# Optimization experiments

Measured on AMD Instinct MI355X. Metric: run time of the kernel, lower is better.

Reference implementation:

```python
import jax, jax.numpy as jnp
import numpy as np


def _gru_cell(x, h, W_ih, W_hh, b_ih, b_hh):
    # torch.nn.GRUCell semantics, gate order (r, z, n)
    gi = x @ W_ih.T + b_ih          # [B, 3H]
    gh = h @ W_hh.T + b_hh          # [B, 3H]
    ir, iz, inn = jnp.split(gi, 3, axis=-1)
    hr, hz, hn = jnp.split(gh, 3, axis=-1)
    r = jax.nn.sigmoid(ir + hr)
    z = jax.nn.sigmoid(iz + hz)
    n = jnp.tanh(inn + r * hn)
    return (1.0 - z) * n + z * h


def setup_inputs() -> dict:
    key = jax.random.key(0)
    ks = jax.random.split(key, 9)
    B, T, X, H = 128, 512, 64, 256
    s = 0.05
    return {
        "input": jax.random.normal(ks[0], (B, T, X), jnp.float32),
        "h_enc": jax.random.normal(ks[1], (B, H), jnp.float32),
        "W_ih": jax.random.normal(ks[2], (3 * H, X), jnp.float32) * s,
        "W_hh": jax.random.normal(ks[3], (3 * H, H), jnp.float32) * s,
        "b_ih": jnp.zeros((3 * H,), jnp.float32),
        "b_hh": jnp.zeros((3 * H,), jnp.float32),
        "W_out": jax.random.normal(ks[4], (X, H), jnp.float32) * s,
        "b_out": jnp.zeros((X,), jnp.float32),
        "mask0": jax.random.randint(ks[5], (T,), 0, 2, jnp.int32),
        "mask1": jax.random.randint(ks[6], (T,), 0, 2, jnp.int32),
        "skip_size": 4,
    }


def _skip_tables(T, skip):
    # Replicates Python-list negative indexing of the original forward.
    # Skip-list position at the GRU call (pre-append):  2i   if i<skip else i-skip
    # Skip-list position at the projection (post-append): 2i+1 if i<skip else i-skip
    # Positions < skip are zero placeholders; position p >= skip is H[p-skip].
    g_idx = np.zeros(T, np.int32); g_zero = np.zeros(T, bool)
    p_idx = np.zeros(T, np.int32); p_zero = np.zeros(T, bool)
    for i in range(T):
        pg = 2 * i if i < skip else i - skip
        pp = 2 * i + 1 if i < skip else i - skip
        g_zero[i] = pg < skip; g_idx[i] = max(pg - skip, 0)
        p_zero[i] = pp < skip; p_idx[i] = max(pp - skip, 0)
    return g_idx, g_zero, p_idx, p_zero


def reference(input, h_enc, W_ih, W_hh, b_ih, b_hh, W_out, b_out, mask0, mask1, skip_size):
    B, T, X = input.shape
    H = h_enc.shape[1]
    g_idx, g_zero, p_idx, p_zero = _skip_tables(T, int(skip_size))
    m0 = mask0.astype(input.dtype)
    m1 = mask1.astype(input.dtype)

    xs = (jnp.arange(T), m0, m1,
          jnp.asarray(g_idx), jnp.asarray(g_zero),
          jnp.asarray(p_idx), jnp.asarray(p_zero))

    def step(carry, sx):
        h_prev, x_prev, buf = carry          # buf: [T, B, H] history of GRU outputs
        i, a0, a1, gi, gz, pi, pz = sx
        skip_g = jnp.where(gz, 0.0, buf[gi])            # [B, H]
        hidden = h_prev * a0 + skip_g * a1
        h_new = _gru_cell(x_prev, hidden, W_ih, W_hh, b_ih, b_hh)
        buf = buf.at[i].set(h_new)                       # append H[i]
        skip_p = jnp.where(pz, 0.0, buf[pi])
        out = (h_prev + skip_p) @ W_out.T + b_out        # [B, X]
        return (h_new, out, buf), out

    buf0 = jnp.zeros((T, B, H), input.dtype)
    go = jnp.zeros((B, X), input.dtype)                  # GO token
    (_, _, _), outs = jax.lax.scan(step, (h_enc, go, buf0), xs)
    return jnp.transpose(outs, (1, 0, 2))                # [B, T, X]
```

## Files before the change

kernel.cpp:

```cpp
#include <hip/hip_runtime.h>

typedef _Float16 h2_t __attribute__((ext_vector_type(2)));

constexpr int T_ = 512;
constexpr int X_ = 64;
constexpr int H_ = 256;
constexpr int NWG = 128;
constexpr int NT = 512;
constexpr int RS = 16;

constexpr int G_TOTAL = 64 * NT;

__device__ __forceinline__ float sigmoid_f(float x) {
  float e = __expf(fminf(-x, 80.f));
  return 1.f / (1.f + e);
}
__device__ __forceinline__ float tanh_f(float x) {
  float e = __expf(fminf(-2.f * x, 80.f));
  return (1.f - e) / (1.f + e);
}

__device__ __forceinline__ unsigned pk2(float a, float b) {
  h2_t v;
  v[0] = (_Float16)a;
  v[1] = (_Float16)b;
  return __builtin_bit_cast(unsigned, v);
}
__device__ __forceinline__ uint4 pk8(const float* s) {
  return make_uint4(pk2(s[0], s[1]), pk2(s[2], s[3]), pk2(s[4], s[5]),
                    pk2(s[6], s[7]));
}

__device__ __forceinline__ float dotp(unsigned w, unsigned h, float acc) {
  h2_t wv = __builtin_bit_cast(h2_t, w);
  h2_t hv = __builtin_bit_cast(h2_t, h);
#if __has_builtin(__builtin_amdgcn_fdot2)
  return __builtin_amdgcn_fdot2(wv, hv, acc, false);
#else
  acc = fmaf((float)wv[0], (float)hv[0], acc);
  return fmaf((float)wv[1], (float)hv[1], acc);
#endif
}
__device__ __forceinline__ float dotq(uint4 w, uint4 h, float acc) {
  acc = dotp(w.x, h.x, acc);
  acc = dotp(w.y, h.y, acc);
  acc = dotp(w.z, h.z, acc);
  acc = dotp(w.w, h.w, acc);
  return acc;
}

__device__ __forceinline__ float dpp_xor1(float x) {
  int v = __builtin_amdgcn_update_dpp(0, __builtin_bit_cast(int, x), 0xB1,
                                      0xF, 0xF, true);
  return __builtin_bit_cast(float, v);
}
__device__ __forceinline__ float dpp_xor2(float x) {
  int v = __builtin_amdgcn_update_dpp(0, __builtin_bit_cast(int, x), 0x4E,
                                      0xF, 0xF, true);
  return __builtin_bit_cast(float, v);
}

__device__ __forceinline__ void bar_lds() {
  asm volatile("s_waitcnt lgkmcnt(0)\n\ts_barrier" ::: "memory");
}

__global__ void prep_kernel(const float* __restrict__ Wih,
                            const float* __restrict__ Whh,
                            const float* __restrict__ Wout,
                            uint4* __restrict__ G) {
  int id = blockIdx.x * 256 + threadIdx.x;
  if (id >= G_TOTAL) return;
  int t = id & (NT - 1), u = id >> 9;
  int c = t >> 1, kh = t & 1;
  if (u < 32) {
    int g = u >> 4, j = u & 15;
    G[id] = pk8(Whh + (size_t)(g * 256 + c) * H_ + kh * 128 + j * 8);
  } else if (u < 48) {
    int j = u - 32;
    G[id] = pk8(Whh + (size_t)(512 + c) * H_ + kh * 128 + j * 8);
  } else if (u < 60) {
    int v = u - 48, g = v >> 2, j = v & 3;
    G[id] = pk8(Wih + (size_t)(g * 256 + c) * X_ + kh * 32 + j * 8);
  } else {
    int j = u - 60, xc = t >> 3, sl = t & 7;
    G[id] = pk8(Wout + (size_t)xc * H_ + sl * 32 + j * 8);
  }
}

#define PTW(cp) (((cp) >> 4) * 36 + ((cp)&15))
#define HIW(w) ((w) + (((w) >> 6) << 2))


#define GATES(p, i, hn)                                                      \
  float hn;                                                                  \
  {                                                                          \
    float a0 = 0, a1 = 0, z0 = 0, z1 = 0, n0 = 0, n1 = 0, ni = 0;            \
    const uint4* h4 = ((const uint4*)hid2[p]) + kh * 17;                     \
    _Pragma("unroll") for (int j = 0; j < 16; j += 2) {                      \
      uint4 ha = h4[j], hb = h4[j + 1];       \
      uint4 wna = wn4[j * NT + t], wnb = wn4[(j + 1) * NT + t];              \
      a0 = dotq(whh_rz[j], ha, a0);                                          \
      a1 = dotq(whh_rz[j + 1], hb, a1);                                      \
      z0 = dotq(whh_rz[16 + j], ha, z0);                                     \
      z1 = dotq(whh_rz[17 + j], hb, z1);                                     \
      n0 = dotq(wna, ha, n0);                                                \
      n1 = dotq(wnb, hb, n1);                                                \
    }                                                                        \
    const uint4* x4 = ((const uint4*)xt2[p]) + kh * 4;                       \
    _Pragma("unroll") for (int j = 0; j < 4; ++j) {                          \
      uint4 xa = x4[j];                                                      \
      a0 = dotq(wih[j], xa, a0);                                             \
      z0 = dotq(wih[4 + j], xa, z0);                                         \
      ni = dotq(wih[8 + j], xa, ni);                                         \
    }                                                                        \
    float ar = a0 + a1, az = z0 + z1, anh = n0 + n1;                         \
    ar += dpp_xor1(ar);                                                      \
    az += dpp_xor1(az);                                                      \
    anh += dpp_xor1(anh);                                                    \
    ni += dpp_xor1(ni);                                                      \
    float r = sigmoid_f(ar + bsr);                                           \
    float z = sigmoid_f(az + bsz);                                           \
    float n = tanh_f(ni + bin_ + r * (anh + bhn_));                          \
    hn = fmaf(z, hid_reg - n, n);                    \
    if (kh == 0) ring[(i) & (RS - 1)][c] = hn;                               \
  }

#define PROJ_FIN(q, i)                                                       \
  {                                                                          \
    fa += dpp_xor1(fa);                                                      \
    fa += dpp_xor2(fa);                                                      \
    fa += __shfl_xor(fa, 4);                                                 \
    float o = fa + bo;                                                       \
    if (sl == 0) out[ob + (size_t)(i)*X_ + xc] = o;                          \
    float oo = __shfl_xor(o, 8);                                             \
    if ((t & 15) == 0) xt2[q][t >> 4] = pk2(o, oo);                          \
  }

#define PROJ(p, q, i)                                                        \
  {                                                                          \
    float fa = 0;                                                            \
    const uint4* p4 = (const uint4*)&pt2[p][sl * 36];                        \
    _Pragma("unroll") for (int j = 0; j < 4; ++j) fa =                       \
        dotq(wout[j], p4[j], fa);                                            \
    PROJ_FIN(q, i)                                                           \
  }

#define MSTEP(i, p, q)                                                       \
  {                                                                          \
    float fa = 0;                                                            \
    const uint4* p4 = (const uint4*)&pt2[p][sl * 36];                        \
    _Pragma("unroll") for (int j = 0; j < 4; ++j) fa =                       \
        dotq(wout[j], p4[j], fa);                                            \
    GATES(p, i, hn)                                                          \
    PROJ_FIN(q, i)                                                           \
    if ((i) + 1 < T_) {                                                      \
      float sgp = ring[((i) + 1 - 2 * skip) & (RS - 1)][c];                  \
      float hidn = m0f[(i) + 1] * hn + m1f[(i) + 1] * sgp;                   \
      float ptn = hn + sgp;                                                  \
      hid_reg = hidn;                                                        \
      float ho = dpp_xor2(hidn);                                             \
      float po = dpp_xor2(ptn);                                              \
      if ((t & 3) == 0) {                                                    \
        int w = t >> 2;                                                      \
        hid2[q][HIW(w)] = pk2(hidn, ho);                                     \
        pt2[q][PTW(w)] = pk2(ptn, po);                                       \
      }                                                                      \
    }                                                                        \
    bar_lds();                                                               \
  }

__global__ __attribute__((amdgpu_flat_work_group_size(NT, NT),
                          amdgpu_waves_per_eu(2, 2))) void decoder_kernel(
    const float* __restrict__ h_enc, const float* __restrict__ b_ih,
    const float* __restrict__ b_hh, const float* __restrict__ b_out,
    const int* __restrict__ mask0, const int* __restrict__ mask1,
    const int* __restrict__ skipp, const uint4* __restrict__ G,
    float* __restrict__ out) {
  __shared__ alignas(16) uint4 wn4[16 * NT];
  __shared__ float ring[RS][H_];
  __shared__ alignas(16) unsigned hid2[2][136];
  __shared__ alignas(16) unsigned pt2[2][8 * 36];
  __shared__ alignas(16) unsigned xt2[2][X_ / 2];
  __shared__ float m0f[T_], m1f[T_];

  const int t = threadIdx.x;
  const int b = blockIdx.x;
  const int c = t >> 1, kh = t & 1;
  const int xc = t >> 3, sl = t & 7;
  const size_t ob = (size_t)b * T_ * X_;

  uint4 whh_rz[32];
  uint4 wih[12];
  uint4 wout[4];
#pragma unroll
  for (int u = 0; u < 32; ++u) whh_rz[u] = G[u * NT + t];
#pragma unroll
  for (int u = 0; u < 12; ++u) wih[u] = G[(48 + u) * NT + t];
#pragma unroll
  for (int u = 0; u < 4; ++u) wout[u] = G[(60 + u) * NT + t];

#pragma unroll
  for (int u = 0; u < 16; ++u) wn4[u * NT + t] = G[(32 + u) * NT + t];
  m0f[t] = (float)mask0[t];
  m1f[t] = (float)mask1[t];

  const int skip = skipp[0];
  const int i0 = (skip == 0) ? T_ : ((2 * skip < T_) ? 2 * skip : T_);

  const float bsr = b_ih[c] + b_hh[c];
  const float bsz = b_ih[H_ + c] + b_hh[H_ + c];
  const float bin_ = b_ih[2 * H_ + c];
  const float bhn_ = b_hh[2 * H_ + c];
  const float bo = b_out[xc];

  float hp = h_enc[(size_t)b * H_ + c];
  float hid_reg = (float)mask0[0] * hp;
  float hps_reg = hp;
  {
    float ho = dpp_xor2(hid_reg);
    if ((t & 3) == 0) hid2[0][HIW(t >> 2)] = pk2(hid_reg, ho);
  }
  if (t < X_ / 2) xt2[0][t] = 0u;
  __syncthreads();

  for (int i = 0; i < i0; ++i) {
    const int p = i & 1, q = p ^ 1;
    GATES(p, i, hn)
    {
      int ppos = (i < skip) ? 2 * i + 1 : i - skip;
      bool pz = ppos < skip;
      int pi = ppos - skip;
      if (pi < 0) pi = 0;
      float sp = pz ? 0.f : ((pi == i) ? hn : ring[pi & (RS - 1)][c]);
      float ptv = hps_reg + sp;
      float po = dpp_xor2(ptv);
      if ((t & 3) == 0) pt2[p][PTW(t >> 2)] = pk2(ptv, po);
    }
    if (i + 1 < T_) {
      int i1 = i + 1;
      int pg = (i1 < skip) ? 2 * i1 : i1 - skip;
      bool gz = pg < skip;
      int gi = pg - skip;
      if (gi < 0) gi = 0;
      if (gi >= i1) gz = true;
      float sg = gz ? 0.f : ((gi == i) ? hn : ring[gi & (RS - 1)][c]);
      float hidn = m0f[i1] * hn + m1f[i1] * sg;
      hid_reg = hidn;
      float ho = dpp_xor2(hidn);
      if ((t & 3) == 0) hid2[q][HIW(t >> 2)] = pk2(hidn, ho);
      if (skip > 0 && i1 >= 2 * skip) {
        float sgp = ring[(i1 - 2 * skip) & (RS - 1)][c];
        float ptn = hn + sgp;
        float po2 = dpp_xor2(ptn);
        if ((t & 3) == 0) pt2[q][PTW(t >> 2)] = pk2(ptn, po2);
      }
    }
    hps_reg = hn;
    __syncthreads();
    PROJ(p, q, i)
    __syncthreads();
  }

#pragma unroll 1
  for (int i = i0; i < T_; i += 2) {
    MSTEP(i, 0, 1)
    MSTEP(i + 1, 1, 0)
  }
}

extern "C" void kernel_launch(void* const* d_in, const int* in_sizes, int n_in,
                              void* d_out, int out_size, void* d_ws,
                              size_t ws_size, hipStream_t stream) {
  (void)in_sizes; (void)n_in; (void)out_size; (void)ws_size;
  const float* h_enc = (const float*)d_in[1];
  const float* W_ih = (const float*)d_in[2];
  const float* W_hh = (const float*)d_in[3];
  const float* b_ih = (const float*)d_in[4];
  const float* b_hh = (const float*)d_in[5];
  const float* W_out = (const float*)d_in[6];
  const float* b_out = (const float*)d_in[7];
  const int* mask0 = (const int*)d_in[8];
  const int* mask1 = (const int*)d_in[9];
  const int* skipp = (const int*)d_in[10];
  float* out = (float*)d_out;
  uint4* G = (uint4*)d_ws;

  prep_kernel<<<dim3(G_TOTAL / 256), dim3(256), 0, stream>>>(W_ih, W_hh,
                                                             W_out, G);
  decoder_kernel<<<dim3(NWG), dim3(NT), 0, stream>>>(
      h_enc, b_ih, b_hh, b_out, mask0, mask1, skipp, G, out);
}
```

Measured before the change: 1.077 ms.

## Double block size to 1024 threads with four-way K-split per hidden unit

Result: slower. 1.187 ms (+10.2%).

```diff
diff --git a/kernel.cpp b/kernel.cpp
--- a/kernel.cpp
+++ b/kernel.cpp
@@ -6,10 +6,10 @@
 constexpr int X_ = 64;
 constexpr int H_ = 256;
 constexpr int NWG = 128;
-constexpr int NT = 512;
+constexpr int NT = 1024;
 constexpr int RS = 16;
 
-constexpr int G_TOTAL = 64 * NT;
+constexpr int G_TOTAL = 32 * NT;
 
 __device__ __forceinline__ float sigmoid_f(float x) {
   float e = __expf(fminf(-x, 80.f));
@@ -59,6 +59,9 @@
                                       0xF, 0xF, true);
   return __builtin_bit_cast(float, v);
 }
+#define QRED(v)                                                              \
+  v += dpp_xor1(v);                                                          \
+  v += dpp_xor2(v);
 
 __device__ __forceinline__ void bar_lds() {
   asm volatile("s_waitcnt lgkmcnt(0)\n\ts_barrier" ::: "memory");
@@ -70,59 +73,64 @@
                             uint4* __restrict__ G) {
   int id = blockIdx.x * 256 + threadIdx.x;
   if (id >= G_TOTAL) return;
-  int t = id & (NT - 1), u = id >> 9;
-  int c = t >> 1, kh = t & 1;
-  if (u < 32) {
-    int g = u >> 4, j = u & 15;
-    G[id] = pk8(Whh + (size_t)(g * 256 + c) * H_ + kh * 128 + j * 8);
-  } else if (u < 48) {
-    int j = u - 32;
-    G[id] = pk8(Whh + (size_t)(512 + c) * H_ + kh * 128 + j * 8);
-  } else if (u < 60) {
-    int v = u - 48, g = v >> 2, j = v & 3;
-    G[id] = pk8(Wih + (size_t)(g * 256 + c) * X_ + kh * 32 + j * 8);
+  int t = id & (NT - 1), u = id >> 10;
+  int c = t >> 2, kq = t & 3;
+  if (u < 16) {
+    int g = u >> 3, j = u & 7;
+    G[id] = pk8(Whh + (size_t)(g * 256 + c) * H_ + kq * 64 + j * 8);
+  } else if (u < 24) {
+    int j = u - 16;
+    G[id] = pk8(Whh + (size_t)(512 + c) * H_ + kq * 64 + j * 8);
+  } else if (u < 30) {
+    int v = u - 24, g = v >> 1, j = v & 1;
+    G[id] = pk8(Wih + (size_t)(g * 256 + c) * X_ + kq * 16 + j * 8);
   } else {
-    int j = u - 60, xc = t >> 3, sl = t & 7;
-    G[id] = pk8(Wout + (size_t)xc * H_ + sl * 32 + j * 8);
-  }
-}
-
-#define PTW(cp) (((cp) >> 4) * 36 + ((cp)&15))
-#define HIW(w) ((w) + (((w) >> 6) << 2))
-
-
-#define GATES(p, i, hn)                                                      \
-  float hn;                                                                  \
-  {                                                                          \
-    float a0 = 0, a1 = 0, z0 = 0, z1 = 0, n0 = 0, n1 = 0, ni = 0;            \
-    const uint4* h4 = ((const uint4*)hid2[p]) + kh * 17;                     \
-    _Pragma("unroll") for (int j = 0; j < 16; j += 2) {                      \
-      uint4 ha = h4[j], hb = h4[j + 1];       \
-      uint4 wna = wn4[j * NT + t], wnb = wn4[(j + 1) * NT + t];              \
-      a0 = dotq(whh_rz[j], ha, a0);                                          \
-      a1 = dotq(whh_rz[j + 1], hb, a1);                                      \
-      z0 = dotq(whh_rz[16 + j], ha, z0);                                     \
-      z1 = dotq(whh_rz[17 + j], hb, z1);                                     \
-      n0 = dotq(wna, ha, n0);                                                \
-      n1 = dotq(wnb, hb, n1);                                                \
+    int j = u - 30, xc = t >> 4, sl = t & 15;
+    G[id] = pk8(Wout + (size_t)xc * H_ + sl * 16 + j * 8);
+  }
+}
+
+#define HW_(k) (((k) >> 6) * 36 + (((k)&63) >> 1))
+#define XW_(k) (((k) >> 4) * 12 + (((k)&15) >> 1))
+
+
+#define GATES_BODY(p, i)                                                     \
+  {                                                                          \
+    float ar = 0, az = 0, an = 0, ni = 0;                                    \
+    const uint4* h4 = ((const uint4*)hid4[p]) + kq * 9;                      \
+    _Pragma("unroll") for (int j = 0; j < 8; ++j) {                          \
+      uint4 hj = h4[j];                                                      \
+      uint4 wnj = wn[j * NT + t];                                            \
+      ar = dotq(wrz[j], hj, ar);                                             \
+      az = dotq(wrz[8 + j], hj, az);                                         \
+      an = dotq(wnj, hj, an);                                                \
     }                                                                        \
-    const uint4* x4 = ((const uint4*)xt2[p]) + kh * 4;                       \
-    _Pragma("unroll") for (int j = 0; j < 4; ++j) {                          \
-      uint4 xa = x4[j];                                                      \
-      a0 = dotq(wih[j], xa, a0);                                             \
-      z0 = dotq(wih[4 + j], xa, z0);                                         \
-      ni = dotq(wih[8 + j], xa, ni);                                         \
+    const uint4* x4 = ((const uint4*)xt4[p]) + kq * 3;                       \
+    {                                                                        \
+      uint4 xa = x4[0], xb = x4[1];                                          \
+      ar = dotq(wih[0], xa, ar);                                             \
+      ar = dotq(wih[1], xb, ar);                                             \
+      az = dotq(wih[2], xa, az);                                             \
+      az = dotq(wih[3], xb, az);                                             \
+      ni = dotq(wih[4], xa, ni);                                             \
+      ni = dotq(wih[5], xb, ni);                                             \
     }                                                                        \
-    float ar = a0 + a1, az = z0 + z1, anh = n0 + n1;                         \
-    ar += dpp_xor1(ar);                                                      \
-    az += dpp_xor1(az);                                                      \
-    anh += dpp_xor1(anh);                                                    \
-    ni += dpp_xor1(ni);                                                      \
+    QRED(ar)                                                                 \
+    QRED(az)                                                                 \
+    QRED(an)                                                                 \
+    QRED(ni)                                                                 \
     float r = sigmoid_f(ar + bsr);                                           \
     float z = sigmoid_f(az + bsz);                                           \
-    float n = tanh_f(ni + bin_ + r * (anh + bhn_));                          \
+    float n = tanh_f(ni + bin_ + r * (an + bhn_));                           \
     hn = fmaf(z, hid_reg - n, n);                    \
-    if (kh == 0) ring[(i) & (RS - 1)][c] = hn;                               \
+    if ((t & 3) == 0) ring[(i) & (RS - 1)][c] = hn;                          \
+  }
+
+#define PROJ_DOTS_BODY(p)                                                    \
+  {                                                                          \
+    const uint4* p4 = (const uint4*)&pt2[p][sl * 12];                        \
+    fa = dotq(wout[0], p4[0], 0.f);                                          \
+    fa = dotq(wout[1], p4[1], fa);                                           \
   }
 
 #define PROJ_FIN(q, i)                                                       \
@@ -130,79 +138,70 @@
     fa += dpp_xor1(fa);                                                      \
     fa += dpp_xor2(fa);                                                      \
     fa += __shfl_xor(fa, 4);                                                 \
+    fa += __shfl_xor(fa, 8);                                                 \
     float o = fa + bo;                                                       \
-    if (sl == 0) out[ob + (size_t)(i)*X_ + xc] = o;                          \
-    float oo = __shfl_xor(o, 8);                                             \
-    if ((t & 15) == 0) xt2[q][t >> 4] = pk2(o, oo);                          \
-  }
-
-#define PROJ(p, q, i)                                                        \
-  {                                                                          \
-    float fa = 0;                                                            \
-    const uint4* p4 = (const uint4*)&pt2[p][sl * 36];                        \
-    _Pragma("unroll") for (int j = 0; j < 4; ++j) fa =                       \
-        dotq(wout[j], p4[j], fa);                                            \
-    PROJ_FIN(q, i)                                                           \
+    if ((t & 15) == 0) out[ob + (size_t)(i)*X_ + xc] = o;                    \
+    float oo = __shfl_xor(o, 16);                                            \
+    if ((t & 31) == 0) xt4[q][XW_(xc)] = pk2(o, oo);                         \
   }
 
 #define MSTEP(i, p, q)                                                       \
   {                                                                          \
-    float fa = 0;                                                            \
-    const uint4* p4 = (const uint4*)&pt2[p][sl * 36];                        \
-    _Pragma("unroll") for (int j = 0; j < 4; ++j) fa =                       \
-        dotq(wout[j], p4[j], fa);                                            \
-    GATES(p, i, hn)                                                          \
+    float hn, fa;                                                            \
+    PROJ_DOTS_BODY(p)                                                        \
+    GATES_BODY(p, i)                                                         \
     PROJ_FIN(q, i)                                                           \
     if ((i) + 1 < T_) {                                                      \
-      float sgp = ring[((i) + 1 - 2 * skip) & (RS - 1)][c];                  \
-      float hidn = m0f[(i) + 1] * hn + m1f[(i) + 1] * sgp;                   \
-      float ptn = hn + sgp;                                                  \
+      float sg = ring[((i) + 1 - 2 * skip) & (RS - 1)][c];                   \
+      float hidn = m0f[(i) + 1] * hn + m1f[(i) + 1] * sg;                    \
+      float ptn = hn + sg;                                                   \
       hid_reg = hidn;                                                        \
-      float ho = dpp_xor2(hidn);                                             \
-      float po = dpp_xor2(ptn);                                              \
-      if ((t & 3) == 0) {                                                    \
-        int w = t >> 2;                                                      \
-        hid2[q][HIW(w)] = pk2(hidn, ho);                                     \
-        pt2[q][PTW(w)] = pk2(ptn, po);                                       \
+      float ho = __shfl_xor(hidn, 4);                                        \
+      float po = __shfl_xor(ptn, 4);                                         \
+      if ((t & 7) == 0) {                                                    \
+        hid4[q][HW_(c)] = pk2(hidn, ho);                                     \
+        pt2[q][XW_(c)] = pk2(ptn, po);                                       \
       }                                                                      \
     }                                                                        \
     bar_lds();                                                               \
   }
 
 __global__ __attribute__((amdgpu_flat_work_group_size(NT, NT),
-                          amdgpu_waves_per_eu(2, 2))) void decoder_kernel(
+                          amdgpu_waves_per_eu(4, 4))) void decoder_kernel(
     const float* __restrict__ h_enc, const float* __restrict__ b_ih,
     const float* __restrict__ b_hh, const float* __restrict__ b_out,
     const int* __restrict__ mask0, const int* __restrict__ mask1,
     const int* __restrict__ skipp, const uint4* __restrict__ G,
     float* __restrict__ out) {
-  __shared__ alignas(16) uint4 wn4[16 * NT];
+  __shared__ alignas(16) uint4 wn[8 * NT];
   __shared__ float ring[RS][H_];
-  __shared__ alignas(16) unsigned hid2[2][136];
-  __shared__ alignas(16) unsigned pt2[2][8 * 36];
-  __shared__ alignas(16) unsigned xt2[2][X_ / 2];
+  __shared__ alignas(16) unsigned hid4[2][144];
+  __shared__ alignas(16) unsigned pt2[2][192];
+  __shared__ alignas(16) unsigned xt4[2][48];
   __shared__ float m0f[T_], m1f[T_];
 
   const int t = threadIdx.x;
   const int b = blockIdx.x;
-  const int c = t >> 1, kh = t & 1;
-  const int xc = t >> 3, sl = t & 7;
+  const int c = t >> 2, kq = t & 3;
+  const int xc = t >> 4, sl = t & 15;
   const size_t ob = (size_t)b * T_ * X_;
 
-  uint4 whh_rz[32];
-  uint4 wih[12];
-  uint4 wout[4];
-#pragma unroll
-  for (int u = 0; u < 32; ++u) whh_rz[u] = G[u * NT + t];
-#pragma unroll
-  for (int u = 0; u < 12; ++u) wih[u] = G[(48 + u) * NT + t];
-#pragma unroll
-  for (int u = 0; u < 4; ++u) wout[u] = G[(60 + u) * NT + t];
-
-#pragma unroll
-  for (int u = 0; u < 16; ++u) wn4[u * NT + t] = G[(32 + u) * NT + t];
-  m0f[t] = (float)mask0[t];
-  m1f[t] = (float)mask1[t];
+  uint4 wrz[16];
+  uint4 wih[6];
+  uint4 wout[2];
+#pragma unroll
+  for (int u = 0; u < 16; ++u) wrz[u] = G[u * NT + t];
+#pragma unroll
+  for (int u = 0; u < 6; ++u) wih[u] = G[(24 + u) * NT + t];
+#pragma unroll
+  for (int u = 0; u < 2; ++u) wout[u] = G[(30 + u) * NT + t];
+
+#pragma unroll
+  for (int u = 0; u < 8; ++u) wn[u * NT + t] = G[(16 + u) * NT + t];
+  if (t < T_) {
+    m0f[t] = (float)mask0[t];
+    m1f[t] = (float)mask1[t];
+  }
 
   const int skip = skipp[0];
   const int i0 = (skip == 0) ? T_ : ((2 * skip < T_) ? 2 * skip : T_);
@@ -217,15 +216,16 @@
   float hid_reg = (float)mask0[0] * hp;
   float hps_reg = hp;
   {
-    float ho = dpp_xor2(hid_reg);
-    if ((t & 3) == 0) hid2[0][HIW(t >> 2)] = pk2(hid_reg, ho);
-  }
-  if (t < X_ / 2) xt2[0][t] = 0u;
+    float ho = __shfl_xor(hid_reg, 4);
+    if ((t & 7) == 0) hid4[0][HW_(c)] = pk2(hid_reg, ho);
+  }
+  if (t < 48) xt4[0][t] = 0u;
   __syncthreads();
 
   for (int i = 0; i < i0; ++i) {
     const int p = i & 1, q = p ^ 1;
-    GATES(p, i, hn)
+    float hn, fa;
+    GATES_BODY(p, i)
     {
       int ppos = (i < skip) ? 2 * i + 1 : i - skip;
       bool pz = ppos < skip;
@@ -233,8 +233,8 @@
       if (pi < 0) pi = 0;
       float sp = pz ? 0.f : ((pi == i) ? hn : ring[pi & (RS - 1)][c]);
       float ptv = hps_reg + sp;
-      float po = dpp_xor2(ptv);
-      if ((t & 3) == 0) pt2[p][PTW(t >> 2)] = pk2(ptv, po);
+      float po = __shfl_xor(ptv, 4);
+      if ((t & 7) == 0) pt2[p][XW_(c)] = pk2(ptv, po);
     }
     if (i + 1 < T_) {
       int i1 = i + 1;
@@ -246,18 +246,19 @@
       float sg = gz ? 0.f : ((gi == i) ? hn : ring[gi & (RS - 1)][c]);
       float hidn = m0f[i1] * hn + m1f[i1] * sg;
       hid_reg = hidn;
-      float ho = dpp_xor2(hidn);
-      if ((t & 3) == 0) hid2[q][HIW(t >> 2)] = pk2(hidn, ho);
+      float ho = __shfl_xor(hidn, 4);
+      if ((t & 7) == 0) hid4[q][HW_(c)] = pk2(hidn, ho);
       if (skip > 0 && i1 >= 2 * skip) {
         float sgp = ring[(i1 - 2 * skip) & (RS - 1)][c];
         float ptn = hn + sgp;
-        float po2 = dpp_xor2(ptn);
-        if ((t & 3) == 0) pt2[q][PTW(t >> 2)] = pk2(ptn, po2);
+        float po2 = __shfl_xor(ptn, 4);
+        if ((t & 7) == 0) pt2[q][XW_(c)] = pk2(ptn, po2);
       }
     }
     hps_reg = hn;
     __syncthreads();
-    PROJ(p, q, i)
+    PROJ_DOTS_BODY(p)
+    PROJ_FIN(q, i)
     __syncthreads();
   }
 
```
